# Optimization experiments

Hardware: AMD Instinct MI355X
Metric: run time of the kernel (lower is better)

## Reference

```python
import jax, jax.numpy as jnp
import numpy as np

EMBED_DIM = 1024
HEADS = 16
HEAD_DIM = EMBED_DIM // HEADS


def setup_inputs() -> dict:
    key = jax.random.key(0)
    ks = jax.random.split(key, 9)
    B, T, C = 4, 4096, EMBED_DIM
    s = 1.0 / np.sqrt(C)
    inp = {
        "x": jax.random.normal(ks[0], (B, T, C), dtype=jnp.float32),
        "Wq": jax.random.normal(ks[1], (C, C), dtype=jnp.float32) * s,
        "bq": jnp.zeros((C,), dtype=jnp.float32),
        "Wk": jax.random.normal(ks[2], (C, C), dtype=jnp.float32) * s,
        "bk": jnp.zeros((C,), dtype=jnp.float32),
        "Wv": jax.random.normal(ks[3], (C, C), dtype=jnp.float32) * s,
        "bv": jnp.zeros((C,), dtype=jnp.float32),
        "Wc": jax.random.normal(ks[4], (C, C), dtype=jnp.float32) * s,
        "bc": jnp.zeros((C,), dtype=jnp.float32),
    }
    return inp


def reference(x, Wq, bq, Wk, bk, Wv, bv, Wc, bc):
    B, T, C = x.shape
    H, D = HEADS, HEAD_DIM
    # projections (torch Linear: x @ W.T + b)
    q = (x @ Wq.T + bq).reshape(B, T, H, D).transpose(0, 2, 1, 3)  # [B,H,T,D]
    k = (x @ Wk.T + bk).reshape(B, T, H, D).transpose(0, 2, 1, 3)
    v = (x @ Wv.T + bv).reshape(B, T, H, D).transpose(0, 2, 1, 3)
    # ELU+1 feature map
    q = jax.nn.elu(q) + 1.0
    k = jax.nn.elu(k) + 1.0
    # kv outer product: [B,H,D,D]
    kv = jnp.einsum("bhtd,bhte->bhde", k, v)
    # normalizer: q @ sum_t k  -> [B,H,T,1]
    k_sum = k.sum(axis=2)  # [B,H,D]
    z = 1.0 / (jnp.einsum("bhtd,bhd->bht", q, k_sum)[..., None] + 1e-6)
    y = jnp.einsum("bhtd,bhde->bhte", q, kv) * z  # [B,H,T,D]
    y = y.transpose(0, 2, 1, 3).reshape(B, T, C)
    return y @ Wc.T + bc
```

## Files before the change

kernel.cpp:

```cpp
#include <hip/hip_runtime.h>
#include <math.h>

#define EMBED 1024
#define HEADS 16
#define HD 64
#define BATCH 4
#define TSEQ 4096
#define BH (BATCH * HEADS)
#define MROWS (BATCH * TSEQ)

typedef _Float16 f16;
typedef __attribute__((ext_vector_type(4))) _Float16 f16x4;
typedef __attribute__((ext_vector_type(8))) _Float16 f16x8;
typedef __attribute__((ext_vector_type(4))) float f32x4;

#define GLOBAL_AS __attribute__((address_space(1)))
#define LDS_AS __attribute__((address_space(3)))

__device__ __forceinline__ float elu1(float v) {
    return v > 0.f ? v + 1.f : __expf(v);
}

__device__ __forceinline__ int swzc(int row, int col, int cols) {
    int g = (col >> 3) ^ (row & 7);
    return row * cols + (g << 3) + (col & 7);
}

__device__ __forceinline__ f16x8 fragld(const f16* t, int row, int k, int cols) {
    return *(const f16x8*)&t[swzc(row, k, cols)];
}

__device__ __forceinline__ f32x4 mfma16(f16x8 a, f16x8 b, f32x4 c) {
    return __builtin_amdgcn_mfma_f32_16x16x32_f16(a, b, c, 0, 0, 0);
}

__device__ __forceinline__ void gld_lds16(const f16* g, f16* l) {
    __builtin_amdgcn_global_load_lds((const GLOBAL_AS void*)g, (LDS_AS void*)l, 16, 0, 0);
}

__global__ __launch_bounds__(256) void zero_kernel(float* __restrict__ p, int n) {
    int i = blockIdx.x * 256 + threadIdx.x;
    if (i < n) p[i] = 0.f;
}

__global__ __launch_bounds__(256) void cvt_x(const float* __restrict__ x, f16* __restrict__ xh) {
    size_t i4 = (size_t)blockIdx.x * 256 + threadIdx.x;
    float4 f = *(const float4*)&x[i4 * 4];
    f16x4 h = {(f16)f.x, (f16)f.y, (f16)f.z, (f16)f.w};
    *(f16x4*)&xh[i4 * 4] = h;
}

__global__ __launch_bounds__(256) void pack_w(
    const float* __restrict__ Wq, const float* __restrict__ Wk,
    const float* __restrict__ Wv, const float* __restrict__ Wc,
    const float* __restrict__ bq, const float* __restrict__ bk,
    const float* __restrict__ bv, const float* __restrict__ bc,
    f16* __restrict__ Wall, float* __restrict__ ball)
{
    int i4 = blockIdx.x * 256 + threadIdx.x;
    int cls = i4 >> 18;
    const float* W = cls == 0 ? Wq : cls == 1 ? Wk : cls == 2 ? Wv : Wc;
    int off = (i4 & 0x3FFFF) * 4;
    float4 f = *(const float4*)&W[off];
    f16x4 h = {(f16)f.x, (f16)f.y, (f16)f.z, (f16)f.w};
    *(f16x4*)&Wall[(size_t)i4 * 4] = h;
    if (i4 < 4096) {
        int c2 = i4 >> 10;
        const float* bb = c2 == 0 ? bq : c2 == 1 ? bk : c2 == 2 ? bv : bc;
        ball[i4] = bb[i4 & 1023];
    }
}

__global__ __launch_bounds__(256) void gemm_qkv(
    const f16* __restrict__ xh, const f16* __restrict__ Wall,
    const float* __restrict__ ball,
    f16* __restrict__ q, f16* __restrict__ kT, f16* __restrict__ vT)
{
    __shared__ __align__(16) f16 As[128 * 64];
    __shared__ __align__(16) f16 Bs[128 * 64];

    const int tid = threadIdx.x, lane = tid & 63, w = tid >> 6;
    const int wr = w >> 1, wc4 = w & 1, l15 = lane & 15, l4 = lane >> 4;
    const int m0 = blockIdx.x * 128;
    const int n0 = blockIdx.y * 128;
    const int cls = n0 >> 10;

    const int gcol = ((lane & 7) ^ (lane >> 3)) << 3;
    const int rsub = lane >> 3;
    const size_t arow = (size_t)(m0 + w * 32 + rsub) * EMBED + gcol;
    const size_t brow = (size_t)(n0 + w * 32 + rsub) * EMBED + gcol;

    f32x4 acc[4][4];
    #pragma unroll
    for (int i = 0; i < 4; ++i)
        #pragma unroll
        for (int j = 0; j < 4; ++j) acc[i][j] = (f32x4){0.f, 0.f, 0.f, 0.f};

    for (int k0 = 0; k0 < EMBED; k0 += 64) {
        #pragma unroll
        for (int c = 0; c < 4; ++c) {
            gld_lds16(&xh[arow + (size_t)c * 8 * EMBED + k0], &As[(w * 4 + c) * 512]);
            gld_lds16(&Wall[brow + (size_t)c * 8 * EMBED + k0], &Bs[(w * 4 + c) * 512]);
        }
        __syncthreads();
        #pragma unroll
        for (int kk = 0; kk < 64; kk += 32) {
            f16x8 af[4], bf[4];
            #pragma unroll
            for (int i = 0; i < 4; ++i)
                af[i] = fragld(As, wr * 64 + i * 16 + l15, kk + l4 * 8, 64);
            #pragma unroll
            for (int j = 0; j < 4; ++j)
                bf[j] = fragld(Bs, wc4 * 64 + j * 16 + l15, kk + l4 * 8, 64);
            #pragma unroll
            for (int i = 0; i < 4; ++i)
                #pragma unroll
                for (int j = 0; j < 4; ++j)
                    acc[i][j] = mfma16(af[i], bf[j], acc[i][j]);
        }
        __syncthreads();
    }

    if (cls == 0) {
        #pragma unroll
        for (int j = 0; j < 4; ++j) {
            int c = n0 + wc4 * 64 + j * 16 + l15;
            float bj = ball[c];
            #pragma unroll
            for (int i = 0; i < 4; ++i) {
                #pragma unroll
                for (int r = 0; r < 4; ++r) {
                    int t = m0 + wr * 64 + i * 16 + l4 * 4 + r;
                    q[(size_t)t * EMBED + c] = (f16)elu1(acc[i][j][r] + bj);
                }
            }
        }
    } else {
        f16* dst = (cls == 1) ? kT : vT;
        const bool act = (cls == 1);
        #pragma unroll
        for (int j = 0; j < 4; ++j) {
            int n = n0 + wc4 * 64 + j * 16 + l15;
            int d = n & 1023;
            float bj = ball[n];
            #pragma unroll
            for (int i = 0; i < 4; ++i) {
                int t = m0 + wr * 64 + i * 16 + l4 * 4;
                f16x4 hv;
                #pragma unroll
                for (int r = 0; r < 4; ++r) {
                    float v = acc[i][j][r] + bj;
                    if (act) v = elu1(v);
                    hv[r] = (f16)v;
                }
                *(f16x4*)&dst[(size_t)d * MROWS + t] = hv;
            }
        }
    }
}

__global__ __launch_bounds__(256) void kv_ksum(
    const f16* __restrict__ kT, const f16* __restrict__ vT,
    float* __restrict__ kvg, float* __restrict__ ksg)
{
    __shared__ __align__(16) f16 kl[64 * 128];
    __shared__ __align__(16) f16 vl[64 * 128];

    const int bh = blockIdx.x, b = bh >> 4, h = bh & 15;
    const int tid = threadIdx.x, lane = tid & 63, w = tid >> 6;
    const int l15 = lane & 15, l4 = lane >> 4;
    const int tbase = b * TSEQ + blockIdx.y * 512;

    f32x4 kvacc[4];
    #pragma unroll
    for (int j = 0; j < 4; ++j) kvacc[j] = (f32x4){0.f, 0.f, 0.f, 0.f};
    float ksacc = 0.f;

    for (int ss = 0; ss < 4; ++ss) {
        const int tg = tbase + ss * 128;
        #pragma unroll
        for (int c = 0; c < 4; ++c) {
            int idx = tid + c * 256;
            int row = idx >> 4, t8 = (idx & 15) << 3;
            f16x8 a = *(const f16x8*)&kT[(size_t)(h * 64 + row) * MROWS + tg + t8];
            *(f16x8*)&kl[swzc(row, t8, 128)] = a;
            f16x8 bb = *(const f16x8*)&vT[(size_t)(h * 64 + row) * MROWS + tg + t8];
            *(f16x8*)&vl[swzc(row, t8, 128)] = bb;
        }
        __syncthreads();
        #pragma unroll
        for (int kk = 0; kk < 128; kk += 32) {
            f16x8 a = fragld(vl, 16 * w + l15, kk + l4 * 8, 128);
            #pragma unroll
            for (int j = 0; j < 4; ++j) {
                f16x8 bfr = fragld(kl, j * 16 + l15, kk + l4 * 8, 128);
                kvacc[j] = mfma16(a, bfr, kvacc[j]);
            }
        }
        {
            int d = tid & 63, qq = tid >> 6;
            #pragma unroll
            for (int t8 = 0; t8 < 32; t8 += 8) {
                f16x8 kv8 = fragld(kl, d, qq * 32 + t8, 128);
                #pragma unroll
                for (int e = 0; e < 8; ++e) ksacc += (float)kv8[e];
            }
        }
        __syncthreads();
    }

    #pragma unroll
    for (int j = 0; j < 4; ++j)
        #pragma unroll
        for (int r = 0; r < 4; ++r)
            atomicAdd(&kvg[(size_t)bh * 4096 +
                           (size_t)(16 * w + l4 * 4 + r) * HD + j * 16 + l15],
                      kvacc[j][r]);
    atomicAdd(&ksg[bh * HD + (tid & 63)], ksacc);
}

__global__ __launch_bounds__(256) void y_kernel(
    const f16* __restrict__ q, const float* __restrict__ kvg,
    const float* __restrict__ ksg, f16* __restrict__ y)
{
    __shared__ __align__(16) f16 qs[128 * 64];
    __shared__ __align__(16) f16 kvs[64 * 64];
    __shared__ __align__(16) f16 ylds[128 * 64];
    __shared__ float kss[64];
    __shared__ float zs[128];

    const int bh = blockIdx.x, b = bh >> 4, h = bh & 15;
    const int tid = threadIdx.x, lane = tid & 63, w = tid >> 6;
    const int l15 = lane & 15, l4 = lane >> 4;
    const int t0g = b * TSEQ + blockIdx.y * 128;

    #pragma unroll
    for (int c = 0; c < 4; ++c) {
        int idx = tid + c * 256;
        int row = idx >> 3, col8 = (idx & 7) << 3;
        f16x8 v = *(const f16x8*)&q[(size_t)(t0g + row) * EMBED + h * 64 + col8];
        *(f16x8*)&qs[swzc(row, col8, 64)] = v;
    }
    #pragma unroll
    for (int c = 0; c < 4; ++c) {
        int idx = tid + c * 256;
        int e = idx >> 4, d4 = (idx & 15) << 2;
        float4 f = *(const float4*)&kvg[(size_t)bh * 4096 + e * 64 + d4];
        f16x4 hv = {(f16)f.x, (f16)f.y, (f16)f.z, (f16)f.w};
        *(f16x4*)&kvs[swzc(e, d4, 64)] = hv;
    }
    if (tid < 64) kss[tid] = ksg[bh * HD + tid];
    __syncthreads();

    {
        int t = tid >> 1, dh = (tid & 1) * 32;
        float s = 0.f;
        #pragma unroll
        for (int d8 = 0; d8 < 32; d8 += 8) {
            f16x8 qv = fragld(qs, t, dh + d8, 64);
            #pragma unroll
            for (int e = 0; e < 8; ++e) s += (float)qv[e] * kss[dh + d8 + e];
        }
        s += __shfl_xor(s, 1);
        if ((tid & 1) == 0) zs[t] = 1.f / (s + 1e-6f);
    }
    __syncthreads();

    f32x4 yacc[8];
    #pragma unroll
    for (int jn = 0; jn < 8; ++jn) yacc[jn] = (f32x4){0.f, 0.f, 0.f, 0.f};
    #pragma unroll
    for (int kk = 0; kk < 64; kk += 32) {
        f16x8 a = fragld(kvs, 16 * w + l15, kk + l4 * 8, 64);
        #pragma unroll
        for (int jn = 0; jn < 8; ++jn) {
            f16x8 bq8 = fragld(qs, jn * 16 + l15, kk + l4 * 8, 64);
            yacc[jn] = mfma16(a, bq8, yacc[jn]);
        }
    }
    #pragma unroll
    for (int jn = 0; jn < 8; ++jn) {
        int t = jn * 16 + l15;
        float z = zs[t];
        int e0 = 16 * w + l4 * 4;
        f16x4 hv;
        #pragma unroll
        for (int r = 0; r < 4; ++r) hv[r] = (f16)(yacc[jn][r] * z);
        *(f16x4*)&ylds[swzc(t, e0, 64)] = hv;
    }
    __syncthreads();

    {
        int row = tid >> 1, eh = (tid & 1) * 32;
        size_t gb = (size_t)(t0g + row) * EMBED + h * 64 + eh;
        #pragma unroll
        for (int c8 = 0; c8 < 32; c8 += 8) {
            f16x8 v = fragld(ylds, row, eh + c8, 64);
            *(f16x8*)&y[gb + c8] = v;
        }
    }
}

__global__ __launch_bounds__(256) void gemm_out(
    const f16* __restrict__ y, const f16* __restrict__ Wall,
    const float* __restrict__ ball, float* __restrict__ out)
{
    __shared__ __align__(16) f16 As[128 * 64];
    __shared__ __align__(16) f16 Bs[128 * 64];

    const int tid = threadIdx.x, lane = tid & 63, w = tid >> 6;
    const int wr = w >> 1, wc4 = w & 1, l15 = lane & 15, l4 = lane >> 4;
    const int m0 = blockIdx.x * 128;
    const int n0 = blockIdx.y * 128;

    const int gcol = ((lane & 7) ^ (lane >> 3)) << 3;
    const int rsub = lane >> 3;
    const size_t arow = (size_t)(m0 + w * 32 + rsub) * EMBED + gcol;
    const size_t brow = (size_t)(3072 + n0 + w * 32 + rsub) * EMBED + gcol;

    f32x4 acc[4][4];
    #pragma unroll
    for (int i = 0; i < 4; ++i)
        #pragma unroll
        for (int j = 0; j < 4; ++j) acc[i][j] = (f32x4){0.f, 0.f, 0.f, 0.f};

    for (int k0 = 0; k0 < EMBED; k0 += 64) {
        #pragma unroll
        for (int c = 0; c < 4; ++c) {
            gld_lds16(&y[arow + (size_t)c * 8 * EMBED + k0], &As[(w * 4 + c) * 512]);
            gld_lds16(&Wall[brow + (size_t)c * 8 * EMBED + k0], &Bs[(w * 4 + c) * 512]);
        }
        __syncthreads();
        #pragma unroll
        for (int kk = 0; kk < 64; kk += 32) {
            f16x8 af[4], bf[4];
            #pragma unroll
            for (int i = 0; i < 4; ++i)
                af[i] = fragld(As, wr * 64 + i * 16 + l15, kk + l4 * 8, 64);
            #pragma unroll
            for (int j = 0; j < 4; ++j)
                bf[j] = fragld(Bs, wc4 * 64 + j * 16 + l15, kk + l4 * 8, 64);
            #pragma unroll
            for (int i = 0; i < 4; ++i)
                #pragma unroll
                for (int j = 0; j < 4; ++j)
                    acc[i][j] = mfma16(af[i], bf[j], acc[i][j]);
        }
        __syncthreads();
    }

    #pragma unroll
    for (int j = 0; j < 4; ++j) {
        int n = n0 + wc4 * 64 + j * 16 + l15;
        float bj = ball[3072 + n];
        #pragma unroll
        for (int i = 0; i < 4; ++i) {
            #pragma unroll
            for (int r = 0; r < 4; ++r) {
                int m = m0 + wr * 64 + i * 16 + l4 * 4 + r;
                out[(size_t)m * EMBED + n] = acc[i][j][r] + bj;
            }
        }
    }
}

extern "C" void kernel_launch(void* const* d_in, const int* in_sizes, int n_in,
                              void* d_out, int out_size, void* d_ws, size_t ws_size,
                              hipStream_t stream) {
    (void)in_sizes; (void)n_in; (void)out_size; (void)ws_size;
    const float* x  = (const float*)d_in[0];
    const float* Wq = (const float*)d_in[1];
    const float* bq = (const float*)d_in[2];
    const float* Wk = (const float*)d_in[3];
    const float* bk = (const float*)d_in[4];
    const float* Wv = (const float*)d_in[5];
    const float* bv = (const float*)d_in[6];
    const float* Wc = (const float*)d_in[7];
    const float* bc = (const float*)d_in[8];
    float* out = (float*)d_out;

    char* W = (char*)d_ws;
    f16* xh   = (f16*)W;
    f16* q_ws = (f16*)(W + 33554432);
    f16* kT   = (f16*)(W + 67108864);
    f16* vT   = (f16*)(W + 100663296);
    f16* Wall = (f16*)(W + 134217728);
    float* ball = (float*)(W + 142606336);
    float* kvg  = (float*)(W + 142622720);
    float* ksg  = (float*)(W + 143671296);

    cvt_x<<<16384, 256, 0, stream>>>(x, xh);
    pack_w<<<4096, 256, 0, stream>>>(Wq, Wk, Wv, Wc, bq, bk, bv, bc, Wall, ball);

    const int nzero = BH * HD * HD + BH * HD;
    zero_kernel<<<(nzero + 255) / 256, 256, 0, stream>>>(kvg, nzero);

    gemm_qkv<<<dim3(128, 24), 256, 0, stream>>>(xh, Wall, ball, q_ws, kT, vT);

    kv_ksum<<<dim3(BH, 8), 256, 0, stream>>>(kT, vT, kvg, ksg);

    y_kernel<<<dim3(BH, TSEQ / 128), 256, 0, stream>>>(q_ws, kvg, ksg, q_ws);

    gemm_out<<<dim3(128, 8), 256, 0, stream>>>(q_ws, Wall, ball, out);
}
```

Before: 236.9 us.

## Use 256x256 double-buffered GEMM tiles with staged prefetch for QKV and output projections

Replaces the 128x128 single-buffered GEMM kernels for the QKV and output projections with 256x256 tiles on 512-thread blocks. Shared memory is double-buffered, and the next K-slice's global-to-LDS loads are interleaved across four sub-phases of MFMA work, using explicit waitcnt, barriers and setprio. Block indices are remapped so groups of blocks share A/B tiles in cache. This aims to hide load latency and raise data reuse per block, at the cost of 128KB of LDS per block, a larger accumulator register footprint and fewer blocks in flight. The output GEMM now launches only 256 blocks.

```diff
diff --git a/kernel.cpp b/kernel.cpp
--- a/kernel.cpp
+++ b/kernel.cpp
@@ -36,6 +36,13 @@
 
 __device__ __forceinline__ void gld_lds16(const f16* g, f16* l) {
     __builtin_amdgcn_global_load_lds((const GLOBAL_AS void*)g, (LDS_AS void*)l, 16, 0, 0);
+}
+
+__device__ __forceinline__ void stage64(f16* tile, const f16* gbase, int k0, int r0,
+                                        int w, int lane) {
+    const f16* src = gbase + (size_t)(r0 + w * 8 + (lane >> 3)) * EMBED + k0 +
+                     (((lane & 7) ^ (lane >> 3)) << 3);
+    gld_lds16(src, tile + (r0 + w * 8) * 64);
 }
 
 __global__ __launch_bounds__(256) void zero_kernel(float* __restrict__ p, int n) {
@@ -71,67 +78,128 @@
     }
 }
 
-__global__ __launch_bounds__(256) void gemm_qkv(
+#define GEMM256_MAINLOOP(AB, BB)                                               \
+    f32x4 acc[8][4];                                                           \
+    _Pragma("unroll") for (int i = 0; i < 8; ++i)                              \
+        _Pragma("unroll") for (int j = 0; j < 4; ++j)                          \
+            acc[i][j] = (f32x4){0.f, 0.f, 0.f, 0.f};                           \
+    _Pragma("unroll") for (int r0 = 0; r0 < 256; r0 += 64)                     \
+        stage64(As[0], AB, 0, r0, w, lane);                                    \
+    _Pragma("unroll") for (int r0 = 0; r0 < 256; r0 += 64)                     \
+        stage64(Bs[0], BB, 0, r0, w, lane);                                    \
+    for (int kt = 0; kt < 16; ++kt) {                                          \
+        const int cur = kt & 1, nxt = cur ^ 1;                                 \
+        const int kn = (kt + 1) * 64;                                          \
+        const f16* cA = As[cur]; const f16* cB = Bs[cur];                      \
+        const bool st = (kt < 15);                                             \
+        f16x8 af[4][2], bf[2][2];                                              \
+                 \
+        if (st) {                                                              \
+            stage64(As[nxt], AB, kn, 0, w, lane);                              \
+            stage64(As[nxt], AB, kn, 64, w, lane);                             \
+            asm volatile("s_waitcnt vmcnt(2)" ::: "memory");                   \
+        } else {                                                               \
+            asm volatile("s_waitcnt vmcnt(0)" ::: "memory");                   \
+        }                                                                      \
+        __builtin_amdgcn_s_barrier();                                          \
+        _Pragma("unroll") for (int mi = 0; mi < 4; ++mi)                       \
+            _Pragma("unroll") for (int kk = 0; kk < 2; ++kk)                   \
+                af[mi][kk] = fragld(cA, R + mi * 16 + l15, kk * 32 + l4 * 8, 64); \
+        _Pragma("unroll") for (int nj = 0; nj < 2; ++nj)                       \
+            _Pragma("unroll") for (int kk = 0; kk < 2; ++kk)                   \
+                bf[nj][kk] = fragld(cB, Cb + nj * 16 + l15, kk * 32 + l4 * 8, 64); \
+        __builtin_amdgcn_s_setprio(1);                                         \
+        _Pragma("unroll") for (int kk = 0; kk < 2; ++kk)                       \
+            _Pragma("unroll") for (int mi = 0; mi < 4; ++mi)                   \
+                _Pragma("unroll") for (int nj = 0; nj < 2; ++nj)               \
+                    acc[mi][nj] = mfma16(af[mi][kk], bf[nj][kk], acc[mi][nj]); \
+        __builtin_amdgcn_s_setprio(0);                                         \
+        __builtin_amdgcn_s_barrier();                                          \
+                          \
+        if (st) {                                                              \
+            stage64(As[nxt], AB, kn, 128, w, lane);                            \
+            stage64(As[nxt], AB, kn, 192, w, lane);                            \
+        }                                                                      \
+        _Pragma("unroll") for (int nj = 0; nj < 2; ++nj)                       \
+            _Pragma("unroll") for (int kk = 0; kk < 2; ++kk)                   \
+                bf[nj][kk] = fragld(cB, Cb + 32 + nj * 16 + l15, kk * 32 + l4 * 8, 64); \
+        __builtin_amdgcn_s_setprio(1);                                         \
+        _Pragma("unroll") for (int kk = 0; kk < 2; ++kk)                       \
+            _Pragma("unroll") for (int mi = 0; mi < 4; ++mi)                   \
+                _Pragma("unroll") for (int nj = 0; nj < 2; ++nj)               \
+                    acc[mi][2 + nj] = mfma16(af[mi][kk], bf[nj][kk], acc[mi][2 + nj]); \
+        __builtin_amdgcn_s_setprio(0);                                         \
+        __builtin_amdgcn_s_barrier();                                          \
+                                       \
+        if (st) {                                                              \
+            stage64(Bs[nxt], BB, kn, 0, w, lane);                              \
+            stage64(Bs[nxt], BB, kn, 64, w, lane);                             \
+        }                                                                      \
+        _Pragma("unroll") for (int mi = 0; mi < 4; ++mi)                       \
+            _Pragma("unroll") for (int kk = 0; kk < 2; ++kk)                   \
+                af[mi][kk] = fragld(cA, R + 64 + mi * 16 + l15, kk * 32 + l4 * 8, 64); \
+        _Pragma("unroll") for (int nj = 0; nj < 2; ++nj)                       \
+            _Pragma("unroll") for (int kk = 0; kk < 2; ++kk)                   \
+                bf[nj][kk] = fragld(cB, Cb + nj * 16 + l15, kk * 32 + l4 * 8, 64); \
+        __builtin_amdgcn_s_setprio(1);                                         \
+        _Pragma("unroll") for (int kk = 0; kk < 2; ++kk)                       \
+            _Pragma("unroll") for (int mi = 0; mi < 4; ++mi)                   \
+                _Pragma("unroll") for (int nj = 0; nj < 2; ++nj)               \
+                    acc[4 + mi][nj] = mfma16(af[mi][kk], bf[nj][kk], acc[4 + mi][nj]); \
+        __builtin_amdgcn_s_setprio(0);                                         \
+        __builtin_amdgcn_s_barrier();                                          \
+                          \
+        if (st) {                                                              \
+            stage64(Bs[nxt], BB, kn, 128, w, lane);                            \
+            stage64(Bs[nxt], BB, kn, 192, w, lane);                            \
+        }                                                                      \
+        _Pragma("unroll") for (int nj = 0; nj < 2; ++nj)                       \
+            _Pragma("unroll") for (int kk = 0; kk < 2; ++kk)                   \
+                bf[nj][kk] = fragld(cB, Cb + 32 + nj * 16 + l15, kk * 32 + l4 * 8, 64); \
+        __builtin_amdgcn_s_setprio(1);                                         \
+        _Pragma("unroll") for (int kk = 0; kk < 2; ++kk)                       \
+            _Pragma("unroll") for (int mi = 0; mi < 4; ++mi)                   \
+                _Pragma("unroll") for (int nj = 0; nj < 2; ++nj)               \
+                    acc[4 + mi][2 + nj] = mfma16(af[mi][kk], bf[nj][kk], acc[4 + mi][2 + nj]); \
+        __builtin_amdgcn_s_setprio(0);                                         \
+        __builtin_amdgcn_s_barrier();                                          \
+    }
+
+__global__ __launch_bounds__(512) void gemm_qkv256(
     const f16* __restrict__ xh, const f16* __restrict__ Wall,
     const float* __restrict__ ball,
     f16* __restrict__ q, f16* __restrict__ kT, f16* __restrict__ vT)
 {
-    __shared__ __align__(16) f16 As[128 * 64];
-    __shared__ __align__(16) f16 Bs[128 * 64];
+    __shared__ __align__(16) f16 As[2][256 * 64];
+    __shared__ __align__(16) f16 Bs[2][256 * 64];
 
     const int tid = threadIdx.x, lane = tid & 63, w = tid >> 6;
-    const int wr = w >> 1, wc4 = w & 1, l15 = lane & 15, l4 = lane >> 4;
-    const int m0 = blockIdx.x * 128;
-    const int n0 = blockIdx.y * 128;
+    const int wr = w >> 2, wc = w & 3;
+    const int l15 = lane & 15, l4 = lane >> 4;
+    const int R = wr * 128, Cb = wc * 64;
+
+    const int orig = blockIdx.x;
+    const int wg = (orig & 7) * 96 + (orig >> 3);
+    const int m0 = (wg & 63) * 256;
+    const int n0 = (wg >> 6) * 256;
     const int cls = n0 >> 10;
 
-    const int gcol = ((lane & 7) ^ (lane >> 3)) << 3;
-    const int rsub = lane >> 3;
-    const size_t arow = (size_t)(m0 + w * 32 + rsub) * EMBED + gcol;
-    const size_t brow = (size_t)(n0 + w * 32 + rsub) * EMBED + gcol;
-
-    f32x4 acc[4][4];
-    #pragma unroll
-    for (int i = 0; i < 4; ++i)
-        #pragma unroll
-        for (int j = 0; j < 4; ++j) acc[i][j] = (f32x4){0.f, 0.f, 0.f, 0.f};
-
-    for (int k0 = 0; k0 < EMBED; k0 += 64) {
-        #pragma unroll
-        for (int c = 0; c < 4; ++c) {
-            gld_lds16(&xh[arow + (size_t)c * 8 * EMBED + k0], &As[(w * 4 + c) * 512]);
-            gld_lds16(&Wall[brow + (size_t)c * 8 * EMBED + k0], &Bs[(w * 4 + c) * 512]);
-        }
-        __syncthreads();
-        #pragma unroll
-        for (int kk = 0; kk < 64; kk += 32) {
-            f16x8 af[4], bf[4];
-            #pragma unroll
-            for (int i = 0; i < 4; ++i)
-                af[i] = fragld(As, wr * 64 + i * 16 + l15, kk + l4 * 8, 64);
-            #pragma unroll
-            for (int j = 0; j < 4; ++j)
-                bf[j] = fragld(Bs, wc4 * 64 + j * 16 + l15, kk + l4 * 8, 64);
-            #pragma unroll
-            for (int i = 0; i < 4; ++i)
-                #pragma unroll
-                for (int j = 0; j < 4; ++j)
-                    acc[i][j] = mfma16(af[i], bf[j], acc[i][j]);
-        }
-        __syncthreads();
-    }
+    const f16* Ab = xh + (size_t)m0 * EMBED;
+    const f16* Bb = Wall + (size_t)n0 * EMBED;
+
+    GEMM256_MAINLOOP(Ab, Bb)
 
     if (cls == 0) {
         #pragma unroll
-        for (int j = 0; j < 4; ++j) {
-            int c = n0 + wc4 * 64 + j * 16 + l15;
+        for (int nj = 0; nj < 4; ++nj) {
+            int c = n0 + Cb + nj * 16 + l15;
             float bj = ball[c];
             #pragma unroll
-            for (int i = 0; i < 4; ++i) {
+            for (int mi = 0; mi < 8; ++mi) {
                 #pragma unroll
                 for (int r = 0; r < 4; ++r) {
-                    int t = m0 + wr * 64 + i * 16 + l4 * 4 + r;
-                    q[(size_t)t * EMBED + c] = (f16)elu1(acc[i][j][r] + bj);
+                    int t = m0 + R + mi * 16 + l4 * 4 + r;
+                    q[(size_t)t * EMBED + c] = (f16)elu1(acc[mi][nj][r] + bj);
                 }
             }
         }
@@ -139,21 +207,58 @@
         f16* dst = (cls == 1) ? kT : vT;
         const bool act = (cls == 1);
         #pragma unroll
-        for (int j = 0; j < 4; ++j) {
-            int n = n0 + wc4 * 64 + j * 16 + l15;
+        for (int nj = 0; nj < 4; ++nj) {
+            int n = n0 + Cb + nj * 16 + l15;
             int d = n & 1023;
             float bj = ball[n];
             #pragma unroll
-            for (int i = 0; i < 4; ++i) {
-                int t = m0 + wr * 64 + i * 16 + l4 * 4;
+            for (int mi = 0; mi < 8; ++mi) {
+                int t = m0 + R + mi * 16 + l4 * 4;
                 f16x4 hv;
                 #pragma unroll
                 for (int r = 0; r < 4; ++r) {
-                    float v = acc[i][j][r] + bj;
+                    float v = acc[mi][nj][r] + bj;
                     if (act) v = elu1(v);
                     hv[r] = (f16)v;
                 }
                 *(f16x4*)&dst[(size_t)d * MROWS + t] = hv;
+            }
+        }
+    }
+}
+
+__global__ __launch_bounds__(512) void gemm_out256(
+    const f16* __restrict__ y, const f16* __restrict__ Wall,
+    const float* __restrict__ ball, float* __restrict__ out)
+{
+    __shared__ __align__(16) f16 As[2][256 * 64];
+    __shared__ __align__(16) f16 Bs[2][256 * 64];
+
+    const int tid = threadIdx.x, lane = tid & 63, w = tid >> 6;
+    const int wr = w >> 2, wc = w & 3;
+    const int l15 = lane & 15, l4 = lane >> 4;
+    const int R = wr * 128, Cb = wc * 64;
+
+    const int orig = blockIdx.x;
+    const int wg = (orig & 7) * 32 + (orig >> 3);
+    const int m0 = (wg & 63) * 256;
+    const int n0 = (wg >> 6) * 256;
+
+    const f16* Ab = y + (size_t)m0 * EMBED;
+    const f16* Bb = Wall + (size_t)(3072 + n0) * EMBED;
+
+    GEMM256_MAINLOOP(Ab, Bb)
+
+    #pragma unroll
+    for (int nj = 0; nj < 4; ++nj) {
+        int n = n0 + Cb + nj * 16 + l15;
+        float bj = ball[3072 + n];
+        #pragma unroll
+        for (int mi = 0; mi < 8; ++mi) {
+            #pragma unroll
+            for (int r = 0; r < 4; ++r) {
+                int m = m0 + R + mi * 16 + l4 * 4 + r;
+                out[(size_t)m * EMBED + n] = acc[mi][nj][r] + bj;
             }
         }
     }
@@ -297,69 +402,6 @@
         for (int c8 = 0; c8 < 32; c8 += 8) {
             f16x8 v = fragld(ylds, row, eh + c8, 64);
             *(f16x8*)&y[gb + c8] = v;
-        }
-    }
-}
-
-__global__ __launch_bounds__(256) void gemm_out(
-    const f16* __restrict__ y, const f16* __restrict__ Wall,
-    const float* __restrict__ ball, float* __restrict__ out)
-{
-    __shared__ __align__(16) f16 As[128 * 64];
-    __shared__ __align__(16) f16 Bs[128 * 64];
-
-    const int tid = threadIdx.x, lane = tid & 63, w = tid >> 6;
-    const int wr = w >> 1, wc4 = w & 1, l15 = lane & 15, l4 = lane >> 4;
-    const int m0 = blockIdx.x * 128;
-    const int n0 = blockIdx.y * 128;
-
-    const int gcol = ((lane & 7) ^ (lane >> 3)) << 3;
-    const int rsub = lane >> 3;
-    const size_t arow = (size_t)(m0 + w * 32 + rsub) * EMBED + gcol;
-    const size_t brow = (size_t)(3072 + n0 + w * 32 + rsub) * EMBED + gcol;
-
-    f32x4 acc[4][4];
-    #pragma unroll
-    for (int i = 0; i < 4; ++i)
-        #pragma unroll
-        for (int j = 0; j < 4; ++j) acc[i][j] = (f32x4){0.f, 0.f, 0.f, 0.f};
-
-    for (int k0 = 0; k0 < EMBED; k0 += 64) {
-        #pragma unroll
-        for (int c = 0; c < 4; ++c) {
-            gld_lds16(&y[arow + (size_t)c * 8 * EMBED + k0], &As[(w * 4 + c) * 512]);
-            gld_lds16(&Wall[brow + (size_t)c * 8 * EMBED + k0], &Bs[(w * 4 + c) * 512]);
-        }
-        __syncthreads();
-        #pragma unroll
-        for (int kk = 0; kk < 64; kk += 32) {
-            f16x8 af[4], bf[4];
-            #pragma unroll
-            for (int i = 0; i < 4; ++i)
-                af[i] = fragld(As, wr * 64 + i * 16 + l15, kk + l4 * 8, 64);
-            #pragma unroll
-            for (int j = 0; j < 4; ++j)
-                bf[j] = fragld(Bs, wc4 * 64 + j * 16 + l15, kk + l4 * 8, 64);
-            #pragma unroll
-            for (int i = 0; i < 4; ++i)
-                #pragma unroll
-                for (int j = 0; j < 4; ++j)
-                    acc[i][j] = mfma16(af[i], bf[j], acc[i][j]);
-        }
-        __syncthreads();
-    }
-
-    #pragma unroll
-    for (int j = 0; j < 4; ++j) {
-        int n = n0 + wc4 * 64 + j * 16 + l15;
-        float bj = ball[3072 + n];
-        #pragma unroll
-        for (int i = 0; i < 4; ++i) {
-            #pragma unroll
-            for (int r = 0; r < 4; ++r) {
-                int m = m0 + wr * 64 + i * 16 + l4 * 4 + r;
-                out[(size_t)m * EMBED + n] = acc[i][j][r] + bj;
-            }
         }
     }
 }
@@ -395,11 +437,11 @@
     const int nzero = BH * HD * HD + BH * HD;
     zero_kernel<<<(nzero + 255) / 256, 256, 0, stream>>>(kvg, nzero);
 
-    gemm_qkv<<<dim3(128, 24), 256, 0, stream>>>(xh, Wall, ball, q_ws, kT, vT);
+    gemm_qkv256<<<768, 512, 0, stream>>>(xh, Wall, ball, q_ws, kT, vT);
 
     kv_ksum<<<dim3(BH, 8), 256, 0, stream>>>(kT, vT, kvg, ksg);
 
     y_kernel<<<dim3(BH, TSEQ / 128), 256, 0, stream>>>(q_ws, kvg, ksg, q_ws);
 
-    gemm_out<<<dim3(128, 8), 256, 0, stream>>>(q_ws, Wall, ball, out);
-}
+    gemm_out256<<<256, 512, 0, stream>>>(q_ws, Wall, ball, out);
+}
```

Result: slower. 287.6 us (+21.4%).

## Fuse prep kernels and remap GEMM blocks for XCD-local L2 reuse

Applied to the files above, without the earlier changes.

Merges the x conversion, weight packing and kv/ksum zeroing into one prep launch, which removes two kernel launches. Both GEMMs switch to a 1D grid whose block index is remapped so that each XCD (selected by blockIdx mod 8) handles a contiguous set of 16 M tiles across the N tiles. The goal is for tiles that share A rows to sit on the same XCD's L2 and be reused there. This assumes round-robin block dispatch across 8 XCDs and a grid size that divides evenly into that mapping.

```diff
diff --git a/kernel.cpp b/kernel.cpp
--- a/kernel.cpp
+++ b/kernel.cpp
@@ -38,36 +38,36 @@
     __builtin_amdgcn_global_load_lds((const GLOBAL_AS void*)g, (LDS_AS void*)l, 16, 0, 0);
 }
 
-__global__ __launch_bounds__(256) void zero_kernel(float* __restrict__ p, int n) {
-    int i = blockIdx.x * 256 + threadIdx.x;
-    if (i < n) p[i] = 0.f;
-}
-
-__global__ __launch_bounds__(256) void cvt_x(const float* __restrict__ x, f16* __restrict__ xh) {
-    size_t i4 = (size_t)blockIdx.x * 256 + threadIdx.x;
-    float4 f = *(const float4*)&x[i4 * 4];
-    f16x4 h = {(f16)f.x, (f16)f.y, (f16)f.z, (f16)f.w};
-    *(f16x4*)&xh[i4 * 4] = h;
-}
-
-__global__ __launch_bounds__(256) void pack_w(
+__global__ __launch_bounds__(256) void prep(
+    const float* __restrict__ x, f16* __restrict__ xh,
     const float* __restrict__ Wq, const float* __restrict__ Wk,
     const float* __restrict__ Wv, const float* __restrict__ Wc,
     const float* __restrict__ bq, const float* __restrict__ bk,
     const float* __restrict__ bv, const float* __restrict__ bc,
-    f16* __restrict__ Wall, float* __restrict__ ball)
+    f16* __restrict__ Wall, float* __restrict__ ball, float* __restrict__ kvz)
 {
-    int i4 = blockIdx.x * 256 + threadIdx.x;
-    int cls = i4 >> 18;
-    const float* W = cls == 0 ? Wq : cls == 1 ? Wk : cls == 2 ? Wv : Wc;
-    int off = (i4 & 0x3FFFF) * 4;
-    float4 f = *(const float4*)&W[off];
-    f16x4 h = {(f16)f.x, (f16)f.y, (f16)f.z, (f16)f.w};
-    *(f16x4*)&Wall[(size_t)i4 * 4] = h;
-    if (i4 < 4096) {
-        int c2 = i4 >> 10;
-        const float* bb = c2 == 0 ? bq : c2 == 1 ? bk : c2 == 2 ? bv : bc;
-        ball[i4] = bb[i4 & 1023];
+    int bid = blockIdx.x;
+    if (bid < 16384) {
+        size_t i4 = (size_t)bid * 256 + threadIdx.x;
+        float4 f = *(const float4*)&x[i4 * 4];
+        f16x4 h = {(f16)f.x, (f16)f.y, (f16)f.z, (f16)f.w};
+        *(f16x4*)&xh[i4 * 4] = h;
+    } else {
+        int i4 = (bid - 16384) * 256 + threadIdx.x;
+        int cls = i4 >> 18;
+        const float* W = cls == 0 ? Wq : cls == 1 ? Wk : cls == 2 ? Wv : Wc;
+        int off = (i4 & 0x3FFFF) * 4;
+        float4 f = *(const float4*)&W[off];
+        f16x4 h = {(f16)f.x, (f16)f.y, (f16)f.z, (f16)f.w};
+        *(f16x4*)&Wall[(size_t)i4 * 4] = h;
+        if (i4 < 4096) {
+            int c2 = i4 >> 10;
+            const float* bb = c2 == 0 ? bq : c2 == 1 ? bk : c2 == 2 ? bv : bc;
+            ball[i4] = bb[i4 & 1023];
+        }
+        if (i4 < 66560) {
+            *(float4*)&kvz[i4 * 4] = (float4){0.f, 0.f, 0.f, 0.f};
+        }
     }
 }
 
@@ -81,8 +81,14 @@
 
     const int tid = threadIdx.x, lane = tid & 63, w = tid >> 6;
     const int wr = w >> 1, wc4 = w & 1, l15 = lane & 15, l4 = lane >> 4;
-    const int m0 = blockIdx.x * 128;
-    const int n0 = blockIdx.y * 128;
+
+    const int orig = blockIdx.x;
+    const int xcd = orig & 7;
+    const int local = orig >> 3;
+    const int ntile = local >> 4;
+    const int mloc = local & 15;
+    const int m0 = (xcd * 16 + mloc) * 128;
+    const int n0 = ntile * 128;
     const int cls = n0 >> 10;
 
     const int gcol = ((lane & 7) ^ (lane >> 3)) << 3;
@@ -310,8 +316,14 @@
 
     const int tid = threadIdx.x, lane = tid & 63, w = tid >> 6;
     const int wr = w >> 1, wc4 = w & 1, l15 = lane & 15, l4 = lane >> 4;
-    const int m0 = blockIdx.x * 128;
-    const int n0 = blockIdx.y * 128;
+
+    const int orig = blockIdx.x;
+    const int xcd = orig & 7;
+    const int local = orig >> 3;
+    const int ntile = local >> 4;
+    const int mloc = local & 15;
+    const int m0 = (xcd * 16 + mloc) * 128;
+    const int n0 = ntile * 128;
 
     const int gcol = ((lane & 7) ^ (lane >> 3)) << 3;
     const int rsub = lane >> 3;
@@ -389,17 +401,14 @@
     float* kvg  = (float*)(W + 142622720);
     float* ksg  = (float*)(W + 143671296);
 
-    cvt_x<<<16384, 256, 0, stream>>>(x, xh);
-    pack_w<<<4096, 256, 0, stream>>>(Wq, Wk, Wv, Wc, bq, bk, bv, bc, Wall, ball);
-
-    const int nzero = BH * HD * HD + BH * HD;
-    zero_kernel<<<(nzero + 255) / 256, 256, 0, stream>>>(kvg, nzero);
-
-    gemm_qkv<<<dim3(128, 24), 256, 0, stream>>>(xh, Wall, ball, q_ws, kT, vT);
+    prep<<<20480, 256, 0, stream>>>(x, xh, Wq, Wk, Wv, Wc, bq, bk, bv, bc,
+                                    Wall, ball, kvg);
+
+    gemm_qkv<<<3072, 256, 0, stream>>>(xh, Wall, ball, q_ws, kT, vT);
 
     kv_ksum<<<dim3(BH, 8), 256, 0, stream>>>(kT, vT, kvg, ksg);
 
     y_kernel<<<dim3(BH, TSEQ / 128), 256, 0, stream>>>(q_ws, kvg, ksg, q_ws);
 
-    gemm_out<<<dim3(128, 8), 256, 0, stream>>>(q_ws, Wall, ball, out);
-}
+    gemm_out<<<1024, 256, 0, stream>>>(q_ws, Wall, ball, out);
+}
```

Result: no change. 241.1 us (+1.8%).
